# Kernel optimization log

Hardware: AMD Instinct MI355X
Metric: run time of the kernel (lower is better)

Reference implementation:

```python
import jax, jax.numpy as jnp
import numpy as np

B, C, H, W = 8, 256, 48, 48
CK = 64  # C // k
WSCALE = 0.3 / np.sqrt(C)  # keep exp(QK^T) finite (original has no 1/sqrt(d) scaling)


def conv1x1(x, w, b):
    # x: (B,C,H,W), w: (O,C,1,1), b: (O,) -> (B,O,H,W)
    return jnp.einsum('bchw,oc->bohw', x, w[:, :, 0, 0]) + b[None, :, None, None]


def setup_inputs() -> dict:
    key = jax.random.key(0)
    ks = jax.random.split(key, 6)
    x = jax.random.normal(ks[0], (B, C, H, W), dtype=jnp.float32)
    qw = jax.random.normal(ks[1], (CK, C, 1, 1), dtype=jnp.float32) * WSCALE
    kw = jax.random.normal(ks[2], (CK, C, 1, 1), dtype=jnp.float32) * WSCALE
    vw = jax.random.normal(ks[3], (C, C, 1, 1), dtype=jnp.float32) * (1.0 / np.sqrt(C))
    gw = jax.random.normal(ks[4], (C, C, 1, 1), dtype=jnp.float32) * (1.0 / np.sqrt(C))
    zk = jnp.zeros((CK,), dtype=jnp.float32)
    zc = jnp.zeros((C,), dtype=jnp.float32)
    return {
        'x': x,
        'query_weight': qw, 'query_bias': zk,
        'key_weight': kw, 'key_bias': zk,
        'value_weight': vw, 'value_bias': zc,
        'gamma_weight': gw, 'gamma_bias': zc,
        'k': 4,
    }


def reference(x, query_weight, query_bias, key_weight, key_bias,
              value_weight, value_bias, gamma_weight, gamma_bias, k):
    b, c, h, w = x.shape
    n = h * w
    q = conv1x1(x, query_weight, query_bias).reshape(b, -1, n)   # (B,Ck,N)
    kk = conv1x1(x, key_weight, key_bias).reshape(b, -1, n)      # (B,Ck,N)
    # energy[b,i,j] = q_i . k_j  (queries on rows, no sqrt(d) scaling)
    energy = jnp.einsum('bci,bcj->bij', q, kk)                   # (B,N,N)
    energy = jnp.exp(energy)
    energy = energy / jnp.sum(energy, axis=2, keepdims=True)     # unnormalized-softmax over keys
    v = conv1x1(x, value_weight, value_bias).reshape(b, c, n)    # (B,C,N)
    # out[b,c,j] = sum_i v[b,c,i] * energy[b,i,j]  (faithful to torch.bmm(V, energy))
    out = jnp.einsum('bci,bij->bcj', v, energy).reshape(b, c, h, w)
    out = conv1x1(out, gamma_weight, gamma_bias)
    return out
```

## Files before the change

kernel.cpp:

```cpp
#include <hip/hip_runtime.h>

#define BATCH 8
#define CIN   256
#define NPIX  2304
#define CKD   64
#define NIT   (NPIX / 16)
#define NIC   (NPIX / 32)
#define NJB   (NPIX / 64)

typedef _Float16 f16;
typedef __attribute__((ext_vector_type(4))) _Float16 f16x4;
typedef __attribute__((ext_vector_type(8))) _Float16 f16x8;
typedef __attribute__((ext_vector_type(4))) float    f32x4;


__global__ __launch_bounds__(256) void cast_w(
    const float* __restrict__ qw, const float* __restrict__ kw,
    const float* __restrict__ vw, const float* __restrict__ gw,
    f16* __restrict__ Wqk, f16* __restrict__ Wv, f16* __restrict__ Wg)
{
    int idx = (blockIdx.x * 256 + threadIdx.x) * 4;
    const float* src;
    f16* dst;
    if (idx < 16384)      { src = qw + idx;           dst = Wqk + idx; }
    else if (idx < 32768) { src = kw + (idx - 16384); dst = Wqk + idx; }
    else if (idx < 98304) { src = vw + (idx - 32768); dst = Wv + (idx - 32768); }
    else                  { src = gw + (idx - 98304); dst = Wg + (idx - 98304); }
    float4 v = *(const float4*)src;
    f16x4 h = { (f16)v.x, (f16)v.y, (f16)v.z, (f16)v.w };
    *(f16x4*)dst = h;
}

__global__ __launch_bounds__(256) void cast_xT(
    const float* __restrict__ x, f16* __restrict__ xT)
{
    __shared__ float s[64][65];
    const int t = threadIdx.x;
    const int n0 = blockIdx.x * 64, c0 = blockIdx.y * 64, b = blockIdx.z;
    const float* xb = x + ((size_t)b * CIN + c0) * NPIX + n0;

    const int cl = t >> 4, ng = (t & 15) * 4;
    #pragma unroll
    for (int p = 0; p < 4; ++p) {
        float4 v = *(const float4*)(xb + (size_t)(cl + 16 * p) * NPIX + ng);
        s[cl + 16 * p][ng + 0] = v.x;
        s[cl + 16 * p][ng + 1] = v.y;
        s[cl + 16 * p][ng + 2] = v.z;
        s[cl + 16 * p][ng + 3] = v.w;
    }
    __syncthreads();
    const int nl = t >> 2, cs = (t & 3) * 16;
    f16 h[16];
    #pragma unroll
    for (int j = 0; j < 16; ++j) h[j] = (f16)s[cs + j][nl];
    f16* gp = &xT[((size_t)b * NPIX + n0 + nl) * CIN + c0 + cs];
    *(f16x8*)gp       = *(f16x8*)&h[0];
    *(f16x8*)(gp + 8) = *(f16x8*)&h[8];
}

__global__ __launch_bounds__(256) void qk_conv_mfma(
    const f16* __restrict__ xT, const f16* __restrict__ Wqk,
    const float* __restrict__ qbias, const float* __restrict__ kbias,
    f16* __restrict__ q_blk, f16* __restrict__ k_blk)
{
    __shared__ __align__(16) f16 us[32 * 136];
    const int t = threadIdx.x, w = t >> 6, lane = t & 63;
    const int quad = lane >> 4, l16 = lane & 15;
    const int wm = w & 1, wn = w >> 1;
    const int n0 = blockIdx.x * 32, b = blockIdx.y;

    const f16* bp = xT + ((size_t)b * NPIX + n0 + 16 * wn + l16) * CIN;
    const f16* ap = Wqk + (size_t)(64 * wm + l16) * CIN;

    f32x4 acc[4];
    #pragma unroll
    for (int mt = 0; mt < 4; ++mt) acc[mt] = (f32x4){0.f, 0.f, 0.f, 0.f};

    #pragma unroll
    for (int kk = 0; kk < CIN; kk += 32) {
        f16x8 bf = *(const f16x8*)(bp + kk + quad * 8);
        #pragma unroll
        for (int mt = 0; mt < 4; ++mt) {
            f16x8 af = *(const f16x8*)(ap + (size_t)mt * 16 * CIN + kk + quad * 8);
            acc[mt] = __builtin_amdgcn_mfma_f32_16x16x32_f16(af, bf, acc[mt], 0, 0, 0);
        }
    }
    const float* bias = wm ? kbias - 64 : qbias;
    #pragma unroll
    for (int mt = 0; mt < 4; ++mt) {
        int ob = 64 * wm + 16 * mt + quad * 4;
        #pragma unroll
        for (int r = 0; r < 4; ++r)
            us[(16 * wn + l16) * 136 + ob + r] = (f16)(acc[mt][r] + bias[ob + r]);
    }
    __syncthreads();
    {
        int ks2 = t >> 7, nt = (t >> 6) & 1, ln = t & 63;
        const f16* usr = &us[(nt * 16 + (ln & 15)) * 136 + ks2 * 32 + (ln >> 4) * 8];
        size_t base = (((size_t)b * NIT + (n0 >> 4) + nt) * 2 + ks2) * 512 + ln * 8;
        *(f16x8*)&q_blk[base] = *(const f16x8*)(usr);
        *(f16x8*)&k_blk[base] = *(const f16x8*)(usr + 64);
    }
}

#define ESL 136
__global__ __launch_bounds__(256) void energy_S(
    const f16* __restrict__ q_blk, const f16* __restrict__ k_blk,
    float* __restrict__ Pred)
{
    __shared__ __align__(16) f16 es[64 * ESL];
    __shared__ float red2[2][128];
    const int t    = threadIdx.x;
    const int w    = t >> 6, lane = t & 63;
    const int quad = lane >> 4, l16 = lane & 15;
    const int j0 = blockIdx.x * 64, i0 = blockIdx.y * 128, b = blockIdx.z;
    const size_t ln8 = (size_t)lane * 8;
    const f16* qb = q_blk + (size_t)b * NIT * 2 * 512 + ln8;

    f32x4 acc[8];
    #pragma unroll
    for (int mt = 0; mt < 8; ++mt) acc[mt] = (f32x4){0.f, 0.f, 0.f, 0.f};

    #pragma unroll
    for (int ks = 0; ks < 2; ++ks) {
        f16x8 bf = *(const f16x8*)(k_blk +
            (((size_t)b * NIT + (j0 >> 4) + w) * 2 + ks) * 512 + ln8);
        #pragma unroll
        for (int mt = 0; mt < 8; ++mt) {
            f16x8 af = *(const f16x8*)(qb + ((size_t)((i0 >> 4) + mt) * 2 + ks) * 512);
            acc[mt] = __builtin_amdgcn_mfma_f32_16x16x32_f16(af, bf, acc[mt], 0, 0, 0);
        }
    }

    #pragma unroll
    for (int mt = 0; mt < 8; ++mt) {
        f16x4 h = { (f16)__expf(acc[mt][0]), (f16)__expf(acc[mt][1]),
                    (f16)__expf(acc[mt][2]), (f16)__expf(acc[mt][3]) };
        *(f16x4*)&es[(16 * w + l16) * ESL + 16 * mt + quad * 4] = h;
    }
    __syncthreads();
    {
        int i = t & 127, jq = t >> 7;
        float s = 0.f;
        #pragma unroll
        for (int jj = 0; jj < 32; ++jj)
            s += (float)es[(jq * 32 + jj) * ESL + i];
        red2[jq][i] = s;
    }
    __syncthreads();
    if (t < 128)
        Pred[((size_t)blockIdx.x * BATCH + b) * NPIX + i0 + t] =
            red2[0][t] + red2[1][t];
}

__global__ __launch_bounds__(256) void reduce_S(
    const float* __restrict__ Pred, float* __restrict__ S)
{
    const size_t BN = (size_t)BATCH * NPIX;
    size_t idx = (size_t)blockIdx.x * 256 + threadIdx.x;
    float s = 0.f;
    #pragma unroll
    for (int jb = 0; jb < NJB; ++jb)
        s += Pred[(size_t)jb * BN + idx];
    S[idx] = s;
}

__global__ __launch_bounds__(256) void v_conv_mfma(
    const f16* __restrict__ xT, const f16* __restrict__ Wv,
    const float* __restrict__ vbias, const float* __restrict__ S,
    f16* __restrict__ u_blk)
{
    __shared__ __align__(16) f16 smem[9216];
    f16* As = smem;
    f16* Bs = smem + 128 * 40;
    f16* us = smem;
    const int t = threadIdx.x, w = t >> 6, lane = t & 63;
    const int quad = lane >> 4, l16 = lane & 15;
    const int wm = w & 1, wn = w >> 1;
    const int i0 = blockIdx.x * 64, c0 = blockIdx.y * 128, b = blockIdx.z;
    const int sub = t >> 2, le = t & 3;
    const f16* srcA = Wv + (size_t)(c0 + sub) * CIN + le * 8;
    const f16* srcB = xT + ((size_t)b * NPIX + i0 + sub) * CIN + le * 8;
    const int ldsw = sub * 40 + le * 8;

    f32x4 acc[4][2];
    #pragma unroll
    for (int mt = 0; mt < 4; ++mt)
        #pragma unroll
        for (int nt = 0; nt < 2; ++nt)
            acc[mt][nt] = (f32x4){0.f, 0.f, 0.f, 0.f};

    for (int kk = 0; kk < CIN; kk += 32) {
        f16x8 ta0 = *(const f16x8*)(srcA + kk);
        f16x8 ta1 = *(const f16x8*)(srcA + (size_t)64 * CIN + kk);
        f16x8 tb0 = *(const f16x8*)(srcB + kk);
        __syncthreads();
        *(f16x8*)&As[ldsw]           = ta0;
        *(f16x8*)&As[64 * 40 + ldsw] = ta1;
        *(f16x8*)&Bs[ldsw]           = tb0;
        __syncthreads();
        f16x8 af[4], bf[2];
        #pragma unroll
        for (int mt = 0; mt < 4; ++mt)
            af[mt] = *(const f16x8*)&As[(64 * wm + 16 * mt + l16) * 40 + quad * 8];
        #pragma unroll
        for (int nt = 0; nt < 2; ++nt)
            bf[nt] = *(const f16x8*)&Bs[(32 * wn + 16 * nt + l16) * 40 + quad * 8];
        #pragma unroll
        for (int mt = 0; mt < 4; ++mt)
            #pragma unroll
            for (int nt = 0; nt < 2; ++nt)
                acc[mt][nt] = __builtin_amdgcn_mfma_f32_16x16x32_f16(
                    af[mt], bf[nt], acc[mt][nt], 0, 0, 0);
    }

    __syncthreads();
    #pragma unroll
    for (int nt = 0; nt < 2; ++nt) {
        int i = 32 * wn + 16 * nt + l16;
        float is = 1.0f / S[(size_t)b * NPIX + i0 + i];
        #pragma unroll
        for (int mt = 0; mt < 4; ++mt)
            #pragma unroll
            for (int r = 0; r < 4; ++r) {
                int c = 64 * wm + 16 * mt + quad * 4 + r;
                us[c * 72 + i] = (f16)((acc[mt][nt][r] + vbias[c0 + c]) * is);
            }
    }
    __syncthreads();
    #pragma unroll
    for (int p = 0; p < 4; ++p) {
        int g  = t + 256 * p;
        int ct = g >> 7, ic = (g >> 6) & 1, ln = g & 63;
        f16x8 v = *(const f16x8*)&us[(ct * 16 + (ln & 15)) * 72 + ic * 32 + (ln >> 4) * 8];
        *(f16x8*)&u_blk[(((size_t)b * 16 + (c0 >> 4) + ct) * NIC + (i0 >> 5) + ic) * 512 + ln * 8] = v;
    }
}

__global__ __launch_bounds__(256) void fused_bmm(
    const f16* __restrict__ q_blk, const f16* __restrict__ k_blk,
    const f16* __restrict__ u_blk, f16* __restrict__ o1T)
{
    __shared__ __align__(16) f16 es[64 * 72];
    const int t = threadIdx.x, w = t >> 6, lane = t & 63;
    const int quad = lane >> 4, l16 = lane & 15;
    const int j0 = blockIdx.x * 64;
    const int ch = blockIdx.y, b = blockIdx.z;
    const size_t ln8 = (size_t)lane * 8;

    const f16* qb = q_blk + (size_t)b * NIT * 2 * 512 + ln8;
    const f16* ub = u_blk + (size_t)b * 16 * NIC * 512 + ln8;

    f16x8 kf[2];
    #pragma unroll
    for (int ks = 0; ks < 2; ++ks)
        kf[ks] = *(const f16x8*)(k_blk +
            (((size_t)b * NIT + (j0 >> 4) + w) * 2 + ks) * 512 + ln8);

    const int CT0 = ch * 8 + 2 * w;

    f32x4 acc[2][4];
    #pragma unroll
    for (int mt = 0; mt < 2; ++mt)
        #pragma unroll
        for (int jt = 0; jt < 4; ++jt)
            acc[mt][jt] = (f32x4){0.f, 0.f, 0.f, 0.f};

    for (int ic = 0; ic < NPIX / 64; ++ic) {
        f32x4 e[4];
        #pragma unroll
        for (int it = 0; it < 4; ++it) e[it] = (f32x4){0.f, 0.f, 0.f, 0.f};
        #pragma unroll
        for (int ks = 0; ks < 2; ++ks)
            #pragma unroll
            for (int it = 0; it < 4; ++it) {
                f16x8 af = *(const f16x8*)(qb + ((size_t)(ic * 4 + it) * 2 + ks) * 512);
                e[it] = __builtin_amdgcn_mfma_f32_16x16x32_f16(af, kf[ks], e[it], 0, 0, 0);
            }
        __syncthreads();
        #pragma unroll
        for (int it = 0; it < 4; ++it) {
            f16x4 h = { (f16)__expf(e[it][0]), (f16)__expf(e[it][1]),
                        (f16)__expf(e[it][2]), (f16)__expf(e[it][3]) };
            *(f16x4*)&es[(16 * w + l16) * 72 + it * 16 + quad * 4] = h;
        }
        __syncthreads();
        #pragma unroll
        for (int isub = 0; isub < 2; ++isub) {
            f16x8 af0 = *(const f16x8*)(ub + ((size_t)(CT0 + 0) * NIC + ic * 2 + isub) * 512);
            f16x8 af1 = *(const f16x8*)(ub + ((size_t)(CT0 + 1) * NIC + ic * 2 + isub) * 512);
            #pragma unroll
            for (int jt = 0; jt < 4; ++jt) {
                f16x8 bf = *(const f16x8*)&es[(16 * jt + l16) * 72 + isub * 32 + quad * 8];
                acc[0][jt] = __builtin_amdgcn_mfma_f32_16x16x32_f16(af0, bf, acc[0][jt], 0, 0, 0);
                acc[1][jt] = __builtin_amdgcn_mfma_f32_16x16x32_f16(af1, bf, acc[1][jt], 0, 0, 0);
            }
        }
    }

    #pragma unroll
    for (int mt = 0; mt < 2; ++mt) {
        int cb = ch * 128 + 32 * w + 16 * mt + quad * 4;
        #pragma unroll
        for (int jt = 0; jt < 4; ++jt) {
            int j = j0 + 16 * jt + l16;
            f16x4 h = { (f16)acc[mt][jt][0], (f16)acc[mt][jt][1],
                        (f16)acc[mt][jt][2], (f16)acc[mt][jt][3] };
            *(f16x4*)&o1T[((size_t)b * NPIX + j) * CIN + cb] = h;
        }
    }
}

__global__ __launch_bounds__(256) void gamma_conv_mfma(
    const f16* __restrict__ o1T, const f16* __restrict__ Wg,
    const float* __restrict__ gbias, float* __restrict__ out)
{
    __shared__ __align__(16) f16 As[128 * 40];
    __shared__ __align__(16) f16 Bs[64 * 40];
    const int t = threadIdx.x, w = t >> 6, lane = t & 63;
    const int quad = lane >> 4, l16 = lane & 15;
    const int wm = w & 1, wn = w >> 1;
    const int j0 = blockIdx.x * 64, o0 = blockIdx.y * 128, b = blockIdx.z;
    const int sub = t >> 2, le = t & 3;
    const f16* srcA = Wg + (size_t)(o0 + sub) * CIN + le * 8;
    const f16* srcB = o1T + ((size_t)b * NPIX + j0 + sub) * CIN + le * 8;
    const int ldsw = sub * 40 + le * 8;

    f32x4 acc[4][2];
    #pragma unroll
    for (int mt = 0; mt < 4; ++mt)
        #pragma unroll
        for (int nt = 0; nt < 2; ++nt)
            acc[mt][nt] = (f32x4){0.f, 0.f, 0.f, 0.f};

    for (int kk = 0; kk < CIN; kk += 32) {
        f16x8 ta0 = *(const f16x8*)(srcA + kk);
        f16x8 ta1 = *(const f16x8*)(srcA + (size_t)64 * CIN + kk);
        f16x8 tb0 = *(const f16x8*)(srcB + kk);
        __syncthreads();
        *(f16x8*)&As[ldsw]           = ta0;
        *(f16x8*)&As[64 * 40 + ldsw] = ta1;
        *(f16x8*)&Bs[ldsw]           = tb0;
        __syncthreads();
        f16x8 af[4], bf[2];
        #pragma unroll
        for (int mt = 0; mt < 4; ++mt)
            af[mt] = *(const f16x8*)&As[(64 * wm + 16 * mt + l16) * 40 + quad * 8];
        #pragma unroll
        for (int nt = 0; nt < 2; ++nt)
            bf[nt] = *(const f16x8*)&Bs[(32 * wn + 16 * nt + l16) * 40 + quad * 8];
        #pragma unroll
        for (int mt = 0; mt < 4; ++mt)
            #pragma unroll
            for (int nt = 0; nt < 2; ++nt)
                acc[mt][nt] = __builtin_amdgcn_mfma_f32_16x16x32_f16(
                    af[mt], bf[nt], acc[mt][nt], 0, 0, 0);
    }

    #pragma unroll
    for (int mt = 0; mt < 4; ++mt)
        #pragma unroll
        for (int r = 0; r < 4; ++r) {
            int o = o0 + 64 * wm + 16 * mt + quad * 4 + r;
            float bv = gbias[o];
            #pragma unroll
            for (int nt = 0; nt < 2; ++nt) {
                int j = j0 + 32 * wn + 16 * nt + l16;
                out[((size_t)b * CIN + o) * NPIX + j] = acc[mt][nt][r] + bv;
            }
        }
}

extern "C" void kernel_launch(void* const* d_in, const int* in_sizes, int n_in,
                              void* d_out, int out_size, void* d_ws, size_t ws_size,
                              hipStream_t stream) {
    const float* x   = (const float*)d_in[0];
    const float* qw  = (const float*)d_in[1];
    const float* qbv = (const float*)d_in[2];
    const float* kw  = (const float*)d_in[3];
    const float* kbv = (const float*)d_in[4];
    const float* vw  = (const float*)d_in[5];
    const float* vbv = (const float*)d_in[6];
    const float* gw  = (const float*)d_in[7];
    const float* gbv = (const float*)d_in[8];
    float* out = (float*)d_out;

    const size_t BCN  = (size_t)BATCH * CIN * NPIX;
    const size_t BN   = (size_t)BATCH * NPIX;
    const size_t BNCK = (size_t)BATCH * NPIX * CKD;

    f16* q_blk = (f16*)d_ws;
    f16* k_blk = q_blk + BNCK;
    f16* u_blk = k_blk + BNCK;
    f16* xT    = u_blk + BCN;
    f16* o1T   = xT + BCN;
    f16* Wqk   = o1T + BCN;
    f16* Wv    = Wqk + 128 * 256;
    f16* Wg    = Wv + 256 * 256;
    float* S   = (float*)(Wg + 256 * 256);
    float* Pred= S + BN;

    cast_w<<<160, 256, 0, stream>>>(qw, kw, vw, gw, Wqk, Wv, Wg);
    cast_xT<<<dim3(NPIX / 64, CIN / 64, BATCH), 256, 0, stream>>>(x, xT);
    qk_conv_mfma<<<dim3(NPIX / 32, BATCH), 256, 0, stream>>>(xT, Wqk, qbv, kbv, q_blk, k_blk);
    energy_S<<<dim3(NPIX / 64, NPIX / 128, BATCH), 256, 0, stream>>>(q_blk, k_blk, Pred);
    reduce_S<<<(int)(BN / 256), 256, 0, stream>>>(Pred, S);
    v_conv_mfma<<<dim3(NPIX / 64, CIN / 128, BATCH), 256, 0, stream>>>(xT, Wv, vbv, S, u_blk);
    fused_bmm<<<dim3(NPIX / 64, 2, BATCH), 256, 0, stream>>>(q_blk, k_blk, u_blk, o1T);
    gamma_conv_mfma<<<dim3(NPIX / 64, CIN / 128, BATCH), 256, 0, stream>>>(o1T, Wg, gbv, out);
}
```

Measured before the change: 207.9 us.

## Halve fused_bmm j-tile, prefetch Q fragments, and use pre-blocked gamma conv

The fused attention kernel now processes 32 output columns per block with 128-row i-chunks, splitting the energy computation across wave pairs. It double-buffers Q fragments in registers so the next chunk's loads overlap the current work. Its output is written through LDS in an MFMA-fragment blocked layout. The gamma weights are cast into the same blocked layout, so the gamma conv reads fragments straight from global memory without LDS staging. The goal is more blocks for occupancy and fewer LDS round-trips, at the cost of recomputing the exp energy twice as often across the j dimension and issuing more global fragment loads.

```diff
diff --git a/kernel.cpp b/kernel.cpp
--- a/kernel.cpp
+++ b/kernel.cpp
@@ -16,19 +16,32 @@
 
 __global__ __launch_bounds__(256) void cast_w(
     const float* __restrict__ qw, const float* __restrict__ kw,
-    const float* __restrict__ vw, const float* __restrict__ gw,
-    f16* __restrict__ Wqk, f16* __restrict__ Wv, f16* __restrict__ Wg)
+    const float* __restrict__ vw, f16* __restrict__ Wqk, f16* __restrict__ Wv)
 {
     int idx = (blockIdx.x * 256 + threadIdx.x) * 4;
     const float* src;
     f16* dst;
     if (idx < 16384)      { src = qw + idx;           dst = Wqk + idx; }
     else if (idx < 32768) { src = kw + (idx - 16384); dst = Wqk + idx; }
-    else if (idx < 98304) { src = vw + (idx - 32768); dst = Wv + (idx - 32768); }
-    else                  { src = gw + (idx - 98304); dst = Wg + (idx - 98304); }
+    else                  { src = vw + (idx - 32768); dst = Wv + (idx - 32768); }
     float4 v = *(const float4*)src;
     f16x4 h = { (f16)v.x, (f16)v.y, (f16)v.z, (f16)v.w };
     *(f16x4*)dst = h;
+}
+
+__global__ __launch_bounds__(256) void cast_wg(
+    const float* __restrict__ gw, f16* __restrict__ Wg_blk)
+{
+    int tid = blockIdx.x * 256 + threadIdx.x;
+    int tile = tid >> 6, ln = tid & 63;
+    int o = (tile >> 3) * 16 + (ln & 15);
+    int c = (tile & 7) * 32 + (ln >> 4) * 8;
+    const float* src = gw + (size_t)o * CIN + c;
+    float4 v0 = *(const float4*)src;
+    float4 v1 = *(const float4*)(src + 4);
+    f16x8 h = { (f16)v0.x, (f16)v0.y, (f16)v0.z, (f16)v0.w,
+                (f16)v1.x, (f16)v1.y, (f16)v1.z, (f16)v1.w };
+    *(f16x8*)&Wg_blk[(size_t)tile * 512 + ln * 8] = h;
 }
 
 __global__ __launch_bounds__(256) void cast_xT(
@@ -239,13 +252,14 @@
 
 __global__ __launch_bounds__(256) void fused_bmm(
     const f16* __restrict__ q_blk, const f16* __restrict__ k_blk,
-    const f16* __restrict__ u_blk, f16* __restrict__ o1T)
-{
-    __shared__ __align__(16) f16 es[64 * 72];
+    const f16* __restrict__ u_blk, f16* __restrict__ o1_blk)
+{
+    __shared__ __align__(16) f16 es[32 * 136];
     const int t = threadIdx.x, w = t >> 6, lane = t & 63;
     const int quad = lane >> 4, l16 = lane & 15;
-    const int j0 = blockIdx.x * 64;
+    const int j0 = blockIdx.x * 32;
     const int ch = blockIdx.y, b = blockIdx.z;
+    const int jtl = w >> 1, ih = w & 1;
     const size_t ln8 = (size_t)lane * 8;
 
     const f16* qb = q_blk + (size_t)b * NIT * 2 * 512 + ln8;
@@ -255,120 +269,121 @@
     #pragma unroll
     for (int ks = 0; ks < 2; ++ks)
         kf[ks] = *(const f16x8*)(k_blk +
-            (((size_t)b * NIT + (j0 >> 4) + w) * 2 + ks) * 512 + ln8);
-
-    const int CT0 = ch * 8 + 2 * w;
-
-    f32x4 acc[2][4];
+            (((size_t)b * NIT + (j0 >> 4) + jtl) * 2 + ks) * 512 + ln8);
+
+    const int CT0 = ch * 8 + w * 2;
+
+    f32x4 acc[2][2];
     #pragma unroll
     for (int mt = 0; mt < 2; ++mt)
         #pragma unroll
-        for (int jt = 0; jt < 4; ++jt)
+        for (int jt = 0; jt < 2; ++jt)
             acc[mt][jt] = (f32x4){0.f, 0.f, 0.f, 0.f};
 
-    for (int ic = 0; ic < NPIX / 64; ++ic) {
+    f16x8 qfA[4][2], qfB[4][2];
+    #pragma unroll
+    for (int it = 0; it < 4; ++it)
+        #pragma unroll
+        for (int ks = 0; ks < 2; ++ks)
+            qfA[it][ks] = *(const f16x8*)(qb + ((size_t)(ih * 4 + it) * 2 + ks) * 512);
+
+    auto body = [&](int ic, f16x8 (&cur)[4][2], f16x8 (&nxt)[4][2]) {
         f32x4 e[4];
         #pragma unroll
         for (int it = 0; it < 4; ++it) e[it] = (f32x4){0.f, 0.f, 0.f, 0.f};
         #pragma unroll
         for (int ks = 0; ks < 2; ++ks)
             #pragma unroll
-            for (int it = 0; it < 4; ++it) {
-                f16x8 af = *(const f16x8*)(qb + ((size_t)(ic * 4 + it) * 2 + ks) * 512);
-                e[it] = __builtin_amdgcn_mfma_f32_16x16x32_f16(af, kf[ks], e[it], 0, 0, 0);
-            }
+            for (int it = 0; it < 4; ++it)
+                e[it] = __builtin_amdgcn_mfma_f32_16x16x32_f16(
+                    cur[it][ks], kf[ks], e[it], 0, 0, 0);
         __syncthreads();
         #pragma unroll
         for (int it = 0; it < 4; ++it) {
             f16x4 h = { (f16)__expf(e[it][0]), (f16)__expf(e[it][1]),
                         (f16)__expf(e[it][2]), (f16)__expf(e[it][3]) };
-            *(f16x4*)&es[(16 * w + l16) * 72 + it * 16 + quad * 4] = h;
+            *(f16x4*)&es[(jtl * 16 + l16) * 136 + ih * 64 + it * 16 + quad * 4] = h;
         }
         __syncthreads();
-        #pragma unroll
-        for (int isub = 0; isub < 2; ++isub) {
-            f16x8 af0 = *(const f16x8*)(ub + ((size_t)(CT0 + 0) * NIC + ic * 2 + isub) * 512);
-            f16x8 af1 = *(const f16x8*)(ub + ((size_t)(CT0 + 1) * NIC + ic * 2 + isub) * 512);
+        if (ic + 1 < NPIX / 128)
             #pragma unroll
-            for (int jt = 0; jt < 4; ++jt) {
-                f16x8 bf = *(const f16x8*)&es[(16 * jt + l16) * 72 + isub * 32 + quad * 8];
-                acc[0][jt] = __builtin_amdgcn_mfma_f32_16x16x32_f16(af0, bf, acc[0][jt], 0, 0, 0);
-                acc[1][jt] = __builtin_amdgcn_mfma_f32_16x16x32_f16(af1, bf, acc[1][jt], 0, 0, 0);
-            }
-        }
-    }
-
-    #pragma unroll
-    for (int mt = 0; mt < 2; ++mt) {
-        int cb = ch * 128 + 32 * w + 16 * mt + quad * 4;
-        #pragma unroll
-        for (int jt = 0; jt < 4; ++jt) {
-            int j = j0 + 16 * jt + l16;
+            for (int it = 0; it < 4; ++it)
+                #pragma unroll
+                for (int ks = 0; ks < 2; ++ks)
+                    nxt[it][ks] = *(const f16x8*)(qb +
+                        ((size_t)((ic + 1) * 8 + ih * 4 + it) * 2 + ks) * 512);
+        #pragma unroll
+        for (int isub = 0; isub < 4; ++isub) {
+            f16x8 bf0 = *(const f16x8*)&es[(l16) * 136 + isub * 32 + quad * 8];
+            f16x8 bf1 = *(const f16x8*)&es[(16 + l16) * 136 + isub * 32 + quad * 8];
+            f16x8 a0 = *(const f16x8*)(ub + ((size_t)(CT0 + 0) * NIC + ic * 4 + isub) * 512);
+            f16x8 a1 = *(const f16x8*)(ub + ((size_t)(CT0 + 1) * NIC + ic * 4 + isub) * 512);
+            acc[0][0] = __builtin_amdgcn_mfma_f32_16x16x32_f16(a0, bf0, acc[0][0], 0, 0, 0);
+            acc[0][1] = __builtin_amdgcn_mfma_f32_16x16x32_f16(a0, bf1, acc[0][1], 0, 0, 0);
+            acc[1][0] = __builtin_amdgcn_mfma_f32_16x16x32_f16(a1, bf0, acc[1][0], 0, 0, 0);
+            acc[1][1] = __builtin_amdgcn_mfma_f32_16x16x32_f16(a1, bf1, acc[1][1], 0, 0, 0);
+        }
+    };
+
+    for (int ic = 0; ic < NPIX / 128; ic += 2) {
+        body(ic, qfA, qfB);
+        body(ic + 1, qfB, qfA);
+    }
+
+    __syncthreads();
+    f16* us = es;
+    #pragma unroll
+    for (int mt = 0; mt < 2; ++mt)
+        #pragma unroll
+        for (int jt = 0; jt < 2; ++jt) {
             f16x4 h = { (f16)acc[mt][jt][0], (f16)acc[mt][jt][1],
                         (f16)acc[mt][jt][2], (f16)acc[mt][jt][3] };
-            *(f16x4*)&o1T[((size_t)b * NPIX + j) * CIN + cb] = h;
-        }
+            *(f16x4*)&us[(jt * 16 + l16) * 136 + w * 32 + mt * 16 + quad * 4] = h;
+        }
+    __syncthreads();
+    #pragma unroll
+    for (int p = 0; p < 2; ++p) {
+        int g = t + 256 * p;
+        int tile = g >> 6, ln = g & 63;
+        int jt2 = tile >> 2, ccl = tile & 3;
+        f16x8 v = *(const f16x8*)&us[(jt2 * 16 + (ln & 15)) * 136 + ccl * 32 + (ln >> 4) * 8];
+        *(f16x8*)&o1_blk[(((size_t)b * NIT + (j0 >> 4) + jt2) * 8 + ch * 4 + ccl) * 512 + ln * 8] = v;
     }
 }
 
 __global__ __launch_bounds__(256) void gamma_conv_mfma(
-    const f16* __restrict__ o1T, const f16* __restrict__ Wg,
+    const f16* __restrict__ o1_blk, const f16* __restrict__ Wg_blk,
     const float* __restrict__ gbias, float* __restrict__ out)
 {
-    __shared__ __align__(16) f16 As[128 * 40];
-    __shared__ __align__(16) f16 Bs[64 * 40];
     const int t = threadIdx.x, w = t >> 6, lane = t & 63;
     const int quad = lane >> 4, l16 = lane & 15;
-    const int wm = w & 1, wn = w >> 1;
-    const int j0 = blockIdx.x * 64, o0 = blockIdx.y * 128, b = blockIdx.z;
-    const int sub = t >> 2, le = t & 3;
-    const f16* srcA = Wg + (size_t)(o0 + sub) * CIN + le * 8;
-    const f16* srcB = o1T + ((size_t)b * NPIX + j0 + sub) * CIN + le * 8;
-    const int ldsw = sub * 40 + le * 8;
-
-    f32x4 acc[4][2];
-    #pragma unroll
-    for (int mt = 0; mt < 4; ++mt)
-        #pragma unroll
-        for (int nt = 0; nt < 2; ++nt)
-            acc[mt][nt] = (f32x4){0.f, 0.f, 0.f, 0.f};
-
-    for (int kk = 0; kk < CIN; kk += 32) {
-        f16x8 ta0 = *(const f16x8*)(srcA + kk);
-        f16x8 ta1 = *(const f16x8*)(srcA + (size_t)64 * CIN + kk);
-        f16x8 tb0 = *(const f16x8*)(srcB + kk);
-        __syncthreads();
-        *(f16x8*)&As[ldsw]           = ta0;
-        *(f16x8*)&As[64 * 40 + ldsw] = ta1;
-        *(f16x8*)&Bs[ldsw]           = tb0;
-        __syncthreads();
-        f16x8 af[4], bf[2];
-        #pragma unroll
-        for (int mt = 0; mt < 4; ++mt)
-            af[mt] = *(const f16x8*)&As[(64 * wm + 16 * mt + l16) * 40 + quad * 8];
-        #pragma unroll
-        for (int nt = 0; nt < 2; ++nt)
-            bf[nt] = *(const f16x8*)&Bs[(32 * wn + 16 * nt + l16) * 40 + quad * 8];
-        #pragma unroll
-        for (int mt = 0; mt < 4; ++mt)
-            #pragma unroll
-            for (int nt = 0; nt < 2; ++nt)
-                acc[mt][nt] = __builtin_amdgcn_mfma_f32_16x16x32_f16(
-                    af[mt], bf[nt], acc[mt][nt], 0, 0, 0);
-    }
-
-    #pragma unroll
-    for (int mt = 0; mt < 4; ++mt)
-        #pragma unroll
-        for (int r = 0; r < 4; ++r) {
-            int o = o0 + 64 * wm + 16 * mt + quad * 4 + r;
-            float bv = gbias[o];
-            #pragma unroll
-            for (int nt = 0; nt < 2; ++nt) {
-                int j = j0 + 32 * wn + 16 * nt + l16;
-                out[((size_t)b * CIN + o) * NPIX + j] = acc[mt][nt][r] + bv;
-            }
-        }
+    const int j0 = blockIdx.x * 64, oh = blockIdx.y, b = blockIdx.z;
+    const size_t ln8 = (size_t)lane * 8;
+    const f16* bb = o1_blk + ((size_t)b * NIT + (j0 >> 4) + w) * 8 * 512 + ln8;
+    const f16* ab = Wg_blk + (size_t)oh * 8 * 8 * 512 + ln8;
+
+    f32x4 acc[8];
+    #pragma unroll
+    for (int ot = 0; ot < 8; ++ot) acc[ot] = (f32x4){0.f, 0.f, 0.f, 0.f};
+
+    #pragma unroll
+    for (int cc = 0; cc < 8; ++cc) {
+        f16x8 bf = *(const f16x8*)(bb + (size_t)cc * 512);
+        #pragma unroll
+        for (int ot = 0; ot < 8; ++ot) {
+            f16x8 af = *(const f16x8*)(ab + ((size_t)ot * 8 + cc) * 512);
+            acc[ot] = __builtin_amdgcn_mfma_f32_16x16x32_f16(af, bf, acc[ot], 0, 0, 0);
+        }
+    }
+
+    const int j = j0 + w * 16 + l16;
+    #pragma unroll
+    for (int ot = 0; ot < 8; ++ot) {
+        int ob = oh * 128 + ot * 16 + quad * 4;
+        #pragma unroll
+        for (int r = 0; r < 4; ++r)
+            out[((size_t)b * CIN + ob + r) * NPIX + j] = acc[ot][r] + gbias[ob + r];
+    }
 }
 
 extern "C" void kernel_launch(void* const* d_in, const int* in_sizes, int n_in,
@@ -389,23 +404,24 @@
     const size_t BN   = (size_t)BATCH * NPIX;
     const size_t BNCK = (size_t)BATCH * NPIX * CKD;
 
-    f16* q_blk = (f16*)d_ws;
-    f16* k_blk = q_blk + BNCK;
-    f16* u_blk = k_blk + BNCK;
-    f16* xT    = u_blk + BCN;
-    f16* o1T   = xT + BCN;
-    f16* Wqk   = o1T + BCN;
-    f16* Wv    = Wqk + 128 * 256;
-    f16* Wg    = Wv + 256 * 256;
-    float* S   = (float*)(Wg + 256 * 256);
-    float* Pred= S + BN;
-
-    cast_w<<<160, 256, 0, stream>>>(qw, kw, vw, gw, Wqk, Wv, Wg);
+    f16* q_blk  = (f16*)d_ws;
+    f16* k_blk  = q_blk + BNCK;
+    f16* u_blk  = k_blk + BNCK;
+    f16* xT     = u_blk + BCN;
+    f16* o1_blk = xT + BCN;
+    f16* Wqk    = o1_blk + BCN;
+    f16* Wv     = Wqk + 128 * 256;
+    f16* Wg_blk = Wv + 256 * 256;
+    float* S    = (float*)(Wg_blk + 256 * 256);
+    float* Pred = S + BN;
+
+    cast_w<<<96, 256, 0, stream>>>(qw, kw, vw, Wqk, Wv);
+    cast_wg<<<32, 256, 0, stream>>>(gw, Wg_blk);
     cast_xT<<<dim3(NPIX / 64, CIN / 64, BATCH), 256, 0, stream>>>(x, xT);
     qk_conv_mfma<<<dim3(NPIX / 32, BATCH), 256, 0, stream>>>(xT, Wqk, qbv, kbv, q_blk, k_blk);
     energy_S<<<dim3(NPIX / 64, NPIX / 128, BATCH), 256, 0, stream>>>(q_blk, k_blk, Pred);
     reduce_S<<<(int)(BN / 256), 256, 0, stream>>>(Pred, S);
     v_conv_mfma<<<dim3(NPIX / 64, CIN / 128, BATCH), 256, 0, stream>>>(xT, Wv, vbv, S, u_blk);
-    fused_bmm<<<dim3(NPIX / 64, 2, BATCH), 256, 0, stream>>>(q_blk, k_blk, u_blk, o1T);
-    gamma_conv_mfma<<<dim3(NPIX / 64, CIN / 128, BATCH), 256, 0, stream>>>(o1T, Wg, gbv, out);
-}
+    fused_bmm<<<dim3(NPIX / 32, 2, BATCH), 256, 0, stream>>>(q_blk, k_blk, u_blk, o1_blk);
+    gamma_conv_mfma<<<dim3(NPIX / 64, 2, BATCH), 256, 0, stream>>>(o1_blk, Wg_blk, gbv, out);
+}
```

New measurement: 237.0 us. 1.14x slower.
